# Kernel tuning notes

Measured on AMD Instinct MI355X. Metric: run time of the kernel, lower is better.

Reference implementation:

```python
import jax, jax.numpy as jnp
import numpy as np

GAMMA = 1.0
BIG = 1e10  # finite stand-in for +inf so gradients stay nan-free


def setup_inputs() -> dict:
    key = jax.random.key(0)
    k1, k2 = jax.random.split(key)
    input_signals = jax.random.normal(k1, (16, 1024), dtype=jnp.float32)  # B x N (equal-length signals)
    ref_signal = jax.random.normal(k2, (1024,), dtype=jnp.float32)        # M
    return {"input_signals": input_signals, "ref_signal": ref_signal}


def _softmin3(a, b, c, gamma):
    z = -jnp.stack([a, b, c], axis=0) / gamma
    return -gamma * jax.nn.logsumexp(z, axis=0)


def _sdtw(D, gamma):
    """Soft-DTW forward DP via anti-diagonal wavefront.
    D: [B, N, M] pairwise squared distances.
    Returns score [B] and padded score matrix R [B, N+1, M+1].
    """
    B, N, M = D.shape
    i_arr = jnp.arange(N + 1)
    # diagonal d holds cells (i, j=d-i); store as vector over i of length N+1
    r0 = jnp.full((B, N + 1), BIG, dtype=D.dtype).at[:, 0].set(0.0)  # d=0: R[0,0]=0
    r1 = jnp.full((B, N + 1), BIG, dtype=D.dtype)                    # d=1: borders = inf

    def shift(x):  # x[:, i] -> x[:, i-1]
        return jnp.concatenate([jnp.full((B, 1), BIG, dtype=x.dtype), x[:, :-1]], axis=1)

    def step(carry, d):
        r_dm2, r_dm1 = carry
        j_arr = d - i_arr
        valid = (i_arr >= 1) & (i_arr <= N) & (j_arr >= 1) & (j_arr <= M)
        i_safe = jnp.clip(i_arr - 1, 0, N - 1)
        j_safe = jnp.clip(j_arr - 1, 0, M - 1)
        Dd = D[:, i_safe, j_safe]  # [B, N+1], D[i-1, j-1] (0-based) = cost at cell (i,j)
        sm = _softmin3(shift(r_dm2), shift(r_dm1), r_dm1, gamma)  # diag, up, left
        rd = jnp.where(valid[None, :], Dd + sm, BIG)
        return (r_dm1, rd), rd

    ds = jnp.arange(2, N + M + 1)
    _, diags = jax.lax.scan(step, (r0, r1), ds)  # [N+M-1, B, N+1]
    full = jnp.concatenate([r0[None], r1[None], diags], axis=0)  # [N+M+1, B, N+1]
    ii, jj = jnp.meshgrid(jnp.arange(N + 1), jnp.arange(M + 1), indexing="ij")
    R = jnp.moveaxis(full[ii + jj, :, ii], -1, 0)  # [B, N+1, M+1]
    score = R[:, N, M]
    return score, R


def reference(input_signals, ref_signal):
    gamma = GAMMA
    # squared-difference cost matrix, B x N x M
    D = (input_signals[:, :, None] - ref_signal[None, None, :]) ** 2
    score, R = _sdtw(D, gamma)
    # gradient matrix E = d(score)/d(D), the soft-DTW alignment matrix
    _, vjp_fn = jax.vjp(lambda Dm: _sdtw(Dm, gamma)[0], D)
    (E,) = vjp_fn(jnp.ones_like(score))
    return score, D, R, E
```

## Files before the change

kernel.cpp:

```cpp
#include <hip/hip_runtime.h>

#define NN 1024
#define MM 1024
#define NB 16
#define BIGF 1.0e10f
#define TP 17
#define NW 8
#define OFS 5
#define CW 16
#define NA 68
#define NGI (OFS * (NW - 1) + NA)

#define SQC 1.2011224087864498f
#define CLOG2E 1.4426950408889634f
#define LN2F 0.6931471805599453f

typedef float f32x4 __attribute__((ext_vector_type(4)));

#define EXP2F(x) __builtin_amdgcn_exp2f(x)
#define LOG2F(x) __builtin_amdgcn_logf(x)

__device__ __forceinline__ float softmin3s(float a, float b, float c) {
  const float mn = fminf(a, fminf(b, c));
  const float mx = fmaxf(a, fmaxf(b, c));
  const float md = __builtin_amdgcn_fmed3f(a, b, c);
  const float s = 1.0f + EXP2F(mn - md) + EXP2F(mn - mx);
  return mn - LOG2F(s);
}

__global__ __launch_bounds__(256) void d_init_kernel(const float* __restrict__ x,
                                                     const float* __restrict__ y,
                                                     float* __restrict__ D) {
  size_t idx = ((size_t)blockIdx.x * blockDim.x + threadIdx.x) * 4;
  int j = (int)(idx & (MM - 1));
  size_t bi = idx >> 10;
  float xi = x[bi];
  const float4 yv = *reinterpret_cast<const float4*>(y + j);
  float t0 = xi - yv.x, t1 = xi - yv.y, t2 = xi - yv.z, t3 = xi - yv.w;
  float4 o;
  o.x = t0 * t0; o.y = t1 * t1; o.z = t2 * t2; o.w = t3 * t3;
  *reinterpret_cast<float4*>(D + idx) = o;
}

__global__ __launch_bounds__(1024) void r_bound_kernel(float* __restrict__ R) {
  int b = blockIdx.x, t = threadIdx.x;
  float* Rb = R + (size_t)b * (NN + 1) * (MM + 1);
  Rb[t + 1] = BIGF;
  Rb[(size_t)(t + 1) * (MM + 1)] = BIGF;
  if (t == 0) Rb[0] = 0.0f;
}

__global__ __launch_bounds__(512) void sdtw_fwd(const float* __restrict__ x,
                                                const float* __restrict__ y,
                                                float* __restrict__ R,
                                                float* __restrict__ score) {
  __shared__ float tile[NW][2112];
  __shared__ float ringR[NW][128];
  const int b = blockIdx.x, t = threadIdx.x;
  const int w = t >> 6, l = t & 63;
  float* __restrict__ Rb = R + (size_t)b * (NN + 1) * (MM + 1);
  const int i1 = 128 * w + 2 * l + 1;
  const float x1 = x[b * NN + i1 - 1] * SQC;
  const float x2 = x[b * NN + i1] * SQC;
  float* tl = &tile[w][33 * l];
  const int wm1 = (w > 0) ? (w - 1) : 0;
  const bool L0 = (l == 0), W0 = (w == 0);
  const bool pub = (l == 63) && (w < NW - 1);
  float c1 = BIGF, c2 = BIGF, m1 = BIGF;
  float dgc = BIGF;
  __syncthreads();
  for (int G = 0; G < NGI; ++G) {
    const int a = G - OFS * w;
    if (a >= 0 && a < NA) {
      const int s0 = a * CW;
      float yw[16], rgm[17];
#pragma unroll
      for (int p = 0; p < 16; ++p) {
        const int jy = s0 + p - l - 1;
        yw[p] = y[(jy >= 0 && jy < MM) ? jy : 0] * SQC;
      }
#pragma unroll
      for (int k = 0; k < 17; ++k) rgm[k] = ringR[wm1][(s0 + k - 1) & 127];
#pragma unroll
      for (int p = 0; p < CW; ++p) {
        const int j = s0 + p - l;
        const bool act = (j >= 1) && (j <= MM);
        const float up_raw = __shfl_up(m1, 1);
        float up = up_raw;
        float dg = dgc;
        if (L0) {
          up = W0 ? BIGF : rgm[p + 1];
          dg = W0 ? ((j == 1) ? 0.0f : BIGF) : ((j == 1) ? BIGF : rgm[p]);
        }
        dgc = up_raw;
        const float yv = yw[p];
        float dv1 = x1 - yv; dv1 *= dv1;
        const float r1 = dv1 + softmin3s(dg, up, c1);
        float dv2 = x2 - yv; dv2 *= dv2;
        const float r2 = dv2 + softmin3s(c1, r1, c2);
        tl[p] = r1;
        tl[16 + p] = r2;
        if (pub && act) ringR[w][j & 127] = r2;
        m1 = act ? r2 : m1;
        c1 = act ? r1 : c1;
        c2 = act ? r2 : c2;
      }
      __builtin_amdgcn_wave_barrier();
#pragma unroll
      for (int g = 0; g < 32; ++g) {
        const int rr = 4 * g + (l >> 4);
        const int sl = l & 15;
        const int col = s0 + sl - (rr >> 1);
        const float v = tile[w][rr * 16 + (rr >> 1) + sl] * LN2F;
        if (col >= 1 && col <= MM)
          Rb[(size_t)(128 * w + 1 + rr) * (MM + 1) + col] = v;
      }
    }
    __syncthreads();
  }
  if (w == NW - 1 && l == 63) score[b] = m1 * LN2F;
}

__global__ __launch_bounds__(1024) void sdtw_bwd(const float* __restrict__ x,
                                                 const float* __restrict__ y,
                                                 const float* __restrict__ R,
                                                 float* __restrict__ E) {
  __shared__ float ypad[3088];
  __shared__ float rbx[4][NN + 2];
  __shared__ float ebx[4][NN + 2];
  __shared__ float tile[NN][TP];
  const int b = blockIdx.x, t = threadIdx.x;
  const int i = t + 1;
  const float* __restrict__ Rb = R + (size_t)b * (NN + 1) * (MM + 1);
  float* __restrict__ Eb = E + (size_t)b * (size_t)NN * MM;
  for (int k = t; k < 3088; k += 1024)
    ypad[k] = (k >= 1025 && k < 1025 + MM) ? y[k - 1025] * SQC : 0.0f;
#pragma unroll
  for (int q = 0; q < 4; ++q) { rbx[q][i] = -BIGF; ebx[q][i] = 0.0f; }
  if (t == NN - 1) {
#pragma unroll
    for (int q = 0; q < 4; ++q) { rbx[q][NN + 1] = -BIGF; ebx[q][NN + 1] = 0.0f; }
  }
  const float xi = x[b * NN + t] * SQC;
  const float xi1 = x[b * NN + ((t + 1 < NN) ? (t + 1) : t)] * SQC;
  const bool seedrow = (i == NN);
  float rt_e = 0.0f, rt_r = -BIGF;
  float dgn_e = 0.0f, dgn_r = -BIGF;
#pragma unroll
  for (int pass = 0; pass < 4; ++pass) {
    const int row = (pass << 8) + (t >> 2);
    const int ir = row + 1;
    const int c4 = (t & 3) << 2;
    const int jb2 = (128 << 4) - ir + c4;
    if (jb2 >= 1 && jb2 + 3 <= MM) {
      const float4 v = *reinterpret_cast<const float4*>(Rb + (size_t)ir * (MM + 1) + jb2);
      tile[row][c4] = v.x * CLOG2E; tile[row][c4 + 1] = v.y * CLOG2E;
      tile[row][c4 + 2] = v.z * CLOG2E; tile[row][c4 + 3] = v.w * CLOG2E;
    } else {
#pragma unroll
      for (int c = 0; c < 4; ++c) {
        const int jc = jb2 + c;
        tile[row][c4 + c] = (jc >= 1 && jc <= MM)
                                ? Rb[(size_t)ir * (MM + 1) + jc] * CLOG2E
                                : -BIGF;
      }
    }
  }
  __syncthreads();
  float yj = ypad[3088 - i];

  for (int K = 128; K >= 0; --K) {
    const int d0 = K << 4;
#pragma unroll
    for (int p = 0; p < 16; ++p) {
      const int s = 15 - p;
      const int d = d0 + s;
      const int j = d - i;
      const bool act = (j >= 1) && (j <= MM);
      const float dn_r = rbx[(s + 1) & 3][i + 1];
      const float dn_e = ebx[(s + 1) & 3][i + 1];
      const float yjm1 = ypad[j + 1024];
      const float rij = tile[t][s];
      float d1 = xi1 - yjm1; d1 *= d1;
      float d2 = xi - yj;    d2 *= d2;
      float d3 = xi1 - yj;   d3 *= d3;
      const float a1 = dn_r - rij - d1;
      const float a2 = rt_r - rij - d2;
      const float a3 = dgn_r - rij - d3;
      float acc = dn_e * EXP2F(a1) + rt_e * EXP2F(a2) + dgn_e * EXP2F(a3);
      if (seedrow && j == MM) acc += 1.0f;
      rbx[s & 3][i] = act ? rij : -BIGF;
      ebx[s & 3][i] = act ? acc : 0.0f;
      tile[t][s] = act ? acc : 0.0f;
      rt_e = act ? acc : 0.0f;
      rt_r = act ? rij : -BIGF;
      dgn_e = dn_e; dgn_r = dn_r;
      yj = yjm1;
      __syncthreads();
    }
#pragma unroll
    for (int pass = 0; pass < 4; ++pass) {
      const int row = (pass << 8) + (t >> 2);
      const int ir = row + 1;
      const int c4 = (t & 3) << 2;
      const int jb2 = d0 - ir + c4;
      float fv[4];
#pragma unroll
      for (int c = 0; c < 4; ++c) fv[c] = tile[row][c4 + c];
      if (jb2 >= 1 && jb2 + 3 <= MM) {
        f32x4 v;
        v[0] = fv[0]; v[1] = fv[1]; v[2] = fv[2]; v[3] = fv[3];
        const float* pp = Eb + (size_t)row * MM + (jb2 - 1);
        asm volatile("global_store_dwordx4 %0, %1, off" ::"v"(pp), "v"(v) : "memory");
      } else if (jb2 + 3 >= 1 && jb2 <= MM) {
#pragma unroll
        for (int c = 0; c < 4; ++c) {
          const int jc = jb2 + c;
          if (jc >= 1 && jc <= MM) Eb[(size_t)row * MM + (jc - 1)] = fv[c];
        }
      }
      const int jn = jb2 - 16;
      if (jn >= 1 && jn + 3 <= MM) {
        const float4 v = *reinterpret_cast<const float4*>(Rb + (size_t)ir * (MM + 1) + jn);
        tile[row][c4] = v.x * CLOG2E; tile[row][c4 + 1] = v.y * CLOG2E;
        tile[row][c4 + 2] = v.z * CLOG2E; tile[row][c4 + 3] = v.w * CLOG2E;
      } else {
#pragma unroll
        for (int c = 0; c < 4; ++c) {
          const int jc = jn + c;
          tile[row][c4 + c] = (jc >= 1 && jc <= MM)
                                  ? Rb[(size_t)ir * (MM + 1) + jc] * CLOG2E
                                  : -BIGF;
        }
      }
    }
    __syncthreads();
  }
}

extern "C" void kernel_launch(void* const* d_in, const int* in_sizes, int n_in,
                              void* d_out, int out_size, void* d_ws, size_t ws_size,
                              hipStream_t stream) {
  const float* x = (const float*)d_in[0];
  const float* y = (const float*)d_in[1];
  float* out = (float*)d_out;
  float* score = out;
  float* D = out + NB;
  float* R = D + (size_t)NB * NN * MM;
  float* E = R + (size_t)NB * (NN + 1) * (MM + 1);

  hipLaunchKernelGGL(d_init_kernel, dim3((NB * NN * MM) / (256 * 4)), dim3(256), 0, stream,
                     x, y, D);
  hipLaunchKernelGGL(r_bound_kernel, dim3(NB), dim3(1024), 0, stream, R);
  hipLaunchKernelGGL(sdtw_fwd, dim3(NB), dim3(512), 0, stream, x, y, R, score);
  hipLaunchKernelGGL(sdtw_bwd, dim3(NB), dim3(1024), 0, stream, x, y, R, E);
}
```

Baseline: 1.273 ms.

## Pass neighbor DP values via wave shuffles and boundary LDS in backward kernel

The backward soft-DTW wavefront now passes the row-below values (E and R) between lanes with __shfl_down, where it used to go through rotating shared arrays. Only the wave-edge lane exchanges through a small double-buffered boundary array. The y values for each 16-diagonal block are also loaded from global memory into a register window, which removes the padded y array from shared memory. This cuts LDS traffic and shared footprint per step, but adds global y loads per block and divergent boundary handling.

```diff
diff --git a/kernel.cpp b/kernel.cpp
--- a/kernel.cpp
+++ b/kernel.cpp
@@ -125,25 +125,19 @@
                                                  const float* __restrict__ y,
                                                  const float* __restrict__ R,
                                                  float* __restrict__ E) {
-  __shared__ float ypad[3088];
-  __shared__ float rbx[4][NN + 2];
-  __shared__ float ebx[4][NN + 2];
   __shared__ float tile[NN][TP];
+  __shared__ float bndE[2][17];
+  __shared__ float bndR[2][17];
   const int b = blockIdx.x, t = threadIdx.x;
   const int i = t + 1;
+  const int k = t >> 6, l = t & 63;
   const float* __restrict__ Rb = R + (size_t)b * (NN + 1) * (MM + 1);
   float* __restrict__ Eb = E + (size_t)b * (size_t)NN * MM;
-  for (int k = t; k < 3088; k += 1024)
-    ypad[k] = (k >= 1025 && k < 1025 + MM) ? y[k - 1025] * SQC : 0.0f;
-#pragma unroll
-  for (int q = 0; q < 4; ++q) { rbx[q][i] = -BIGF; ebx[q][i] = 0.0f; }
-  if (t == NN - 1) {
-#pragma unroll
-    for (int q = 0; q < 4; ++q) { rbx[q][NN + 1] = -BIGF; ebx[q][NN + 1] = 0.0f; }
-  }
+  if (t < 34) { (&bndE[0][0])[t] = 0.0f; (&bndR[0][0])[t] = -BIGF; }
   const float xi = x[b * NN + t] * SQC;
   const float xi1 = x[b * NN + ((t + 1 < NN) ? (t + 1) : t)] * SQC;
   const bool seedrow = (i == NN);
+  const bool L63 = (l == 63), L0 = (l == 0);
   float rt_e = 0.0f, rt_r = -BIGF;
   float dgn_e = 0.0f, dgn_r = -BIGF;
 #pragma unroll
@@ -167,34 +161,39 @@
     }
   }
   __syncthreads();
-  float yj = ypad[3088 - i];
 
   for (int K = 128; K >= 0; --K) {
     const int d0 = K << 4;
+    float yw[17];
+#pragma unroll
+    for (int u = 0; u < 17; ++u) {
+      const int idx = d0 - i - 1 + u;
+      yw[u] = (idx >= 0 && idx < MM) ? y[idx] * SQC : 0.0f;
+    }
+    float yj = yw[16];
 #pragma unroll
     for (int p = 0; p < 16; ++p) {
       const int s = 15 - p;
       const int d = d0 + s;
       const int j = d - i;
       const bool act = (j >= 1) && (j <= MM);
-      const float dn_r = rbx[(s + 1) & 3][i + 1];
-      const float dn_e = ebx[(s + 1) & 3][i + 1];
-      const float yjm1 = ypad[j + 1024];
+      const int rp = (d + 1) & 1, wp = d & 1;
+      float dn_e = __shfl_down(rt_e, 1);
+      float dn_r = __shfl_down(rt_r, 1);
+      if (L63) { dn_e = bndE[rp][k + 1]; dn_r = bndR[rp][k + 1]; }
+      const float yjm1 = yw[s];
       const float rij = tile[t][s];
       float d1 = xi1 - yjm1; d1 *= d1;
       float d2 = xi - yj;    d2 *= d2;
       float d3 = xi1 - yj;   d3 *= d3;
-      const float a1 = dn_r - rij - d1;
-      const float a2 = rt_r - rij - d2;
-      const float a3 = dgn_r - rij - d3;
-      float acc = dn_e * EXP2F(a1) + rt_e * EXP2F(a2) + dgn_e * EXP2F(a3);
+      float acc = dn_e * EXP2F(dn_r - rij - d1) + rt_e * EXP2F(rt_r - rij - d2) +
+                  dgn_e * EXP2F(dgn_r - rij - d3);
       if (seedrow && j == MM) acc += 1.0f;
-      rbx[s & 3][i] = act ? rij : -BIGF;
-      ebx[s & 3][i] = act ? acc : 0.0f;
       tile[t][s] = act ? acc : 0.0f;
       rt_e = act ? acc : 0.0f;
       rt_r = act ? rij : -BIGF;
       dgn_e = dn_e; dgn_r = dn_r;
+      if (L0 && k > 0) { bndE[wp][k] = rt_e; bndR[wp][k] = rt_r; }
       yj = yjm1;
       __syncthreads();
     }
```

New measurement: 1.551 ms. +21.8%, slower.
